# Optimization experiments

Hardware: AMD Instinct MI355X
Metric: run time of the kernel (lower is better)

Reference implementation:

```python
import jax, jax.numpy as jnp
import numpy as np

N_BINS = 64  # number of piecewise-linear bins; bins vector has N_BINS+1 boundaries
BATCH = 1_000_000


def setup_inputs() -> dict:
    key = jax.random.key(0)
    kx, kb = jax.random.split(key)
    x = jax.random.normal(kx, (BATCH, 1), dtype=jnp.float32)
    # sorted quantile-like boundaries (what adapt() would produce via np.quantile)
    bins = jnp.sort(jax.random.normal(kb, (N_BINS + 1,), dtype=jnp.float32))
    return {"x": x, "bins": bins}


def reference(x, bins):
    # x: [B, 1]; bins: [n_bins+1] sorted boundaries (lookup_table keys 0..n_bins)
    n_bins = bins.shape[0] - 1
    b_lo = bins[:-1]            # boundary[i-1] for bin i=1..n_bins -> [n_bins]
    b_hi = bins[1:]             # boundary[i]                      -> [n_bins]
    idx = jnp.arange(n_bins)    # i-1 in the original loop (i runs 1..n_bins)

    # left_mask_i  = (x < b[i-1]) & (i > 1)        -> idx > 0
    # right_mask_i = (x >= b[i])  & (i < n_bins)   -> idx < n_bins-1
    left = (x < b_lo) & (idx > 0)                  # [B, n_bins]
    right = (x >= b_hi) & (idx < n_bins - 1)       # [B, n_bins]
    v = (x - b_lo) / (b_hi - b_lo)                 # [B, n_bins]

    other = left == right                          # both False inside the bin
    enc = jnp.where(left, 0.0, 1.0)
    enc = jnp.where(other, v, enc)
    return enc.reshape(-1, 1, n_bins)              # [B, 1, n_bins]
```

## Files before the change

### kernel.cpp

```cpp
#include <hip/hip_runtime.h>
#include <float.h>

#define NB 64

typedef float vfloat4 __attribute__((ext_vector_type(4)));

__global__ __launch_bounds__(256) void ple_kernel(const float* __restrict__ x,
                                                  const float* __restrict__ bins,
                                                  float* __restrict__ out,
                                                  long long total4) {
    __shared__ __align__(16) float s_rinv[NB];
    __shared__ __align__(16) float s_nlor[NB];
    __shared__ __align__(16) float s_cl[NB];
    __shared__ __align__(16) float s_ch[NB];

    const int tid = threadIdx.x;
    if (tid < NB) {
        const float lo   = bins[tid];
        const float hi   = bins[tid + 1];
        const float rinv = 1.0f / (hi - lo);
        s_rinv[tid] = rinv;
        s_nlor[tid] = -lo * rinv;
        s_cl[tid] = (tid == 0)      ? -FLT_MAX : 0.0f;
        s_ch[tid] = (tid == NB - 1) ?  FLT_MAX : 1.0f;
    }
    __syncthreads();

    const int j4 = (tid & 15) << 2;
    const vfloat4 rinv4 = *(const vfloat4*)&s_rinv[j4];
    const vfloat4 nlor4 = *(const vfloat4*)&s_nlor[j4];
    const vfloat4 cl4   = *(const vfloat4*)&s_cl[j4];
    const vfloat4 ch4   = *(const vfloat4*)&s_ch[j4];

    const long long base = (long long)blockIdx.x * 1024 + tid;

    long long t[4];
    float xv[4];
#pragma unroll
    for (int k = 0; k < 4; ++k) {
        t[k] = base + (long long)(k << 8);
        xv[k] = (t[k] < total4) ? x[t[k] >> 4] : 0.0f;
    }

#pragma unroll
    for (int k = 0; k < 4; ++k) {
        vfloat4 r;
#pragma unroll
        for (int c = 0; c < 4; ++c) {
            const float v = fmaf(xv[k], rinv4[c], nlor4[c]);
            r[c] = fminf(fmaxf(v, cl4[c]), ch4[c]);
        }
        if (t[k] < total4)
            *((vfloat4*)out + t[k]) = r;
    }
}

extern "C" void kernel_launch(void* const* d_in, const int* in_sizes, int n_in,
                              void* d_out, int out_size, void* d_ws, size_t ws_size,
                              hipStream_t stream) {
    const float* x    = (const float*)d_in[0];
    const float* bins = (const float*)d_in[1];
    float* out        = (float*)d_out;

    const int batch = in_sizes[0];
    const long long total4 = (long long)batch * (NB / 4);
    const long long grid = (total4 + 1023) / 1024;

    ple_kernel<<<(dim3)(unsigned)grid, 256, 0, stream>>>(x, bins, out, total4);
}
```

Measured before the change: 246.2 us.

## Use persistent grid-stride blocks with prefetched x loads and 32-bit indexing

Caps the grid at 2048 blocks and makes each block loop over chunks with a grid stride. Inside the loop it loads the next chunk's x values before computing and storing the current one, so load latency can overlap with the stores. Index arithmetic moves from 64-bit to 32-bit. This amortises the per-block shared-memory bin setup across many chunks. The risk is lower occupancy or fewer stores in flight than the original launch of about 15.6k blocks, and the 32-bit indices cap the supported size.

```diff
diff --git a/kernel.cpp b/kernel.cpp
--- a/kernel.cpp
+++ b/kernel.cpp
@@ -8,7 +8,7 @@
 __global__ __launch_bounds__(256) void ple_kernel(const float* __restrict__ x,
                                                   const float* __restrict__ bins,
                                                   float* __restrict__ out,
-                                                  long long total4) {
+                                                  unsigned total4) {
     __shared__ __align__(16) float s_rinv[NB];
     __shared__ __align__(16) float s_nlor[NB];
     __shared__ __align__(16) float s_cl[NB];
@@ -32,26 +32,42 @@
     const vfloat4 cl4   = *(const vfloat4*)&s_cl[j4];
     const vfloat4 ch4   = *(const vfloat4*)&s_ch[j4];
 
-    const long long base = (long long)blockIdx.x * 1024 + tid;
+    const unsigned step = (unsigned)gridDim.x << 10;
+    unsigned base = ((unsigned)blockIdx.x << 10) + (unsigned)tid;
 
-    long long t[4];
     float xv[4];
 #pragma unroll
     for (int k = 0; k < 4; ++k) {
-        t[k] = base + (long long)(k << 8);
-        xv[k] = (t[k] < total4) ? x[t[k] >> 4] : 0.0f;
+        const unsigned t = base + (unsigned)(k << 8);
+        xv[k] = (t < total4) ? x[t >> 4] : 0.0f;
     }
 
+    while (base < total4) {
+        const unsigned nbase = base + step;
+
+        float xn[4];
 #pragma unroll
-    for (int k = 0; k < 4; ++k) {
-        vfloat4 r;
+        for (int k = 0; k < 4; ++k) {
+            const unsigned t = nbase + (unsigned)(k << 8);
+            xn[k] = (t < total4) ? x[t >> 4] : 0.0f;
+        }
+
 #pragma unroll
-        for (int c = 0; c < 4; ++c) {
-            const float v = fmaf(xv[k], rinv4[c], nlor4[c]);
-            r[c] = fminf(fmaxf(v, cl4[c]), ch4[c]);
+        for (int k = 0; k < 4; ++k) {
+            const unsigned t = base + (unsigned)(k << 8);
+            vfloat4 r;
+#pragma unroll
+            for (int c = 0; c < 4; ++c) {
+                const float v = fmaf(xv[k], rinv4[c], nlor4[c]);
+                r[c] = fminf(fmaxf(v, cl4[c]), ch4[c]);
+            }
+            if (t < total4)
+                *((vfloat4*)out + t) = r;
         }
-        if (t[k] < total4)
-            *((vfloat4*)out + t[k]) = r;
+
+#pragma unroll
+        for (int k = 0; k < 4; ++k) xv[k] = xn[k];
+        base = nbase;
     }
 }
 
@@ -63,8 +79,9 @@
     float* out        = (float*)d_out;
 
     const int batch = in_sizes[0];
-    const long long total4 = (long long)batch * (NB / 4);
-    const long long grid = (total4 + 1023) / 1024;
+    const unsigned total4 = (unsigned)batch * (NB / 4);
+    const unsigned chunks = (total4 + 1023) / 1024;
+    const unsigned grid = chunks < 2048u ? chunks : 2048u;
 
-    ple_kernel<<<(dim3)(unsigned)grid, 256, 0, stream>>>(x, bins, out, total4);
+    ple_kernel<<<(dim3)grid, 256, 0, stream>>>(x, bins, out, total4);
 }
```

New measurement: 250.5 us. No clear change (+1.7%).
